# Kernel optimization log

Measured on AMD Instinct MI355X. Metric: run time of the kernel, lower is better.

Reference implementation:

```python
import jax, jax.numpy as jnp
import numpy as np

LOWER_T = 6.0
UPPER_T = 50.0


def _conv(x, w, pad_h, pad_w):
    # x: [N,1,H,W] or [N,Cin,H,W]; w: [O,I,kh,kw]; cross-correlation like torch Conv2d
    return jax.lax.conv_general_dilated(
        x, w, window_strides=(1, 1),
        padding=[(pad_h, pad_h), (pad_w, pad_w)],
        dimension_numbers=('NCHW', 'OIHW', 'NCHW'))


def setup_inputs() -> dict:
    key = jax.random.key(0)
    H = W = 4096
    img = jax.random.uniform(key, (1, 3, H, W), dtype=jnp.float32) * 255.0

    # scipy.signal.gaussian(5, std=1.0), unnormalized window
    std = 1.0
    g = np.exp(-0.5 * ((np.arange(5, dtype=np.float32) - 2.0) / std) ** 2).astype(np.float32)
    gauss = jnp.asarray(g)  # [5]

    sobel = jnp.asarray(np.array([[1, 0, -1], [2, 0, -2], [1, 0, -1]], dtype=np.float32))  # [3,3]

    f = np.zeros((8, 1, 3, 3), dtype=np.float32)
    f[:, 0, 1, 1] = 1.0
    offs = [(1, 2), (2, 2), (2, 1), (2, 0), (1, 0), (0, 0), (0, 1), (0, 2)]  # 0,45,...,315 deg
    for k, (r, c) in enumerate(offs):
        f[k, 0, r, c] = -1.0
    dir_w = jnp.asarray(f)  # [8,1,3,3]

    return {"img": img, "gauss": gauss, "sobel": sobel, "dir_w": dir_w}


def reference(img, gauss, sobel, dir_w):
    N, C, H, W = img.shape  # N == 1, C == 3
    x = img.reshape(C, 1, H, W)  # treat channels as batch

    # separable gaussian blur: 1x5 then 5x1, padding 2 (matches torch Conv2d)
    gw_h = gauss.reshape(1, 1, 1, 5)
    gw_v = gauss.reshape(1, 1, 5, 1)
    blurred = _conv(_conv(x, gw_h, 0, 2), gw_v, 2, 0)  # [3,1,H,W]

    sw_h = sobel.reshape(1, 1, 3, 3)
    sw_v = sobel.T.reshape(1, 1, 3, 3)
    gx = _conv(blurred, sw_h, 1, 1)  # [3,1,H,W]
    gy = _conv(blurred, sw_v, 1, 1)

    # per-channel magnitude summed over RGB -> [1,1,H,W]
    grad_mag = jnp.sqrt(gx * gx + gy * gy + 1e-8).sum(axis=0, keepdims=True)[:, 0:1]

    gx_sum = gx.sum(axis=0, keepdims=True)[:, 0:1]
    gy_sum = gy.sum(axis=0, keepdims=True)[:, 0:1]
    ori = jnp.arctan2(gy_sum, gx_sum) * (180.0 / 3.14159) + 180.0
    ori = jnp.round(ori / 45.0) * 45.0

    all_filtered = _conv(grad_mag, dir_w, 1, 1)  # [1,8,H,W]

    idx_pos = jnp.mod(ori / 45.0, 8.0).astype(jnp.int32)          # [1,1,H,W]
    idx_neg = jnp.mod(ori / 45.0 + 4.0, 8.0).astype(jnp.int32)

    cs_pos = jnp.take_along_axis(all_filtered, idx_pos, axis=1)  # [1,1,H,W]
    cs_neg = jnp.take_along_axis(all_filtered, idx_neg, axis=1)

    is_max = jnp.minimum(cs_pos, cs_neg) > 0.0

    thin = jnp.where(is_max, grad_mag, 0.0)
    keep = is_max & (thin >= LOWER_T) & (thin <= UPPER_T)
    thresholded = jnp.where(keep, 1.0, 0.0).astype(jnp.float32)  # [1,1,H,W]
    return thresholded
```

## Files before the change

### kernel.cpp

```cpp
#include <hip/hip_runtime.h>


#define IMG_H 4096
#define IMG_W 4096

constexpr int TW = 32, TH = 32;
constexpr int HBH = 40, HBW = 40;
constexpr int BH  = 36, BW  = 40;
constexpr int MH  = 34, MW  = 36;

__global__ __launch_bounds__(256, 6)
void canny_fused(const float* __restrict__ img,
                 const float* __restrict__ gauss,
                 float* __restrict__ out) {
  __shared__ float s_hb[HBH * HBW];
  __shared__ float s_bl[BH * BW];
  __shared__ float s_bs[BH * BW];
  __shared__ float s_mg[MH * MW];

  const int tid = threadIdx.x;
  const int X0 = blockIdx.x * TW;
  const int Y0 = blockIdx.y * TH;

  const float g0 = gauss[0], g1 = gauss[1], g2 = gauss[2],
              g3 = gauss[3], g4 = gauss[4];

  for (int ch = 0; ch < 3; ++ch) {
    const float* im = img + (size_t)ch * ((size_t)IMG_H * IMG_W);

    for (int j = tid; j < HBH * 10; j += 256) {
      int r = j / 10, g = j - r * 10;
      int c0 = g * 4;
      int gy = Y0 - 4 + r;
      float4 o;
      if ((unsigned)gy < IMG_H) {
        int cb = X0 - 4 + c0;
        const float* row = im + (size_t)gy * IMG_W;
        float a0, a1, a2, a3, a4, a5, a6, a7;
        if (cb >= 0 && cb + 7 < IMG_W) {
          float4 va = *(const float4*)(row + cb);
          float4 vb = *(const float4*)(row + cb + 4);
          a0 = va.x; a1 = va.y; a2 = va.z; a3 = va.w;
          a4 = vb.x; a5 = vb.y; a6 = vb.z; a7 = vb.w;
        } else {
          float t[8];
#pragma unroll
          for (int u = 0; u < 8; ++u) {
            int x = cb + u;
            t[u] = ((unsigned)x < IMG_W) ? row[x] : 0.f;
          }
          a0 = t[0]; a1 = t[1]; a2 = t[2]; a3 = t[3];
          a4 = t[4]; a5 = t[5]; a6 = t[6]; a7 = t[7];
        }
        o.x = g0 * a0 + g1 * a1 + g2 * a2 + g3 * a3 + g4 * a4;
        o.y = g0 * a1 + g1 * a2 + g2 * a3 + g3 * a4 + g4 * a5;
        o.z = g0 * a2 + g1 * a3 + g2 * a4 + g3 * a5 + g4 * a6;
        o.w = g0 * a3 + g1 * a4 + g2 * a5 + g3 * a6 + g4 * a7;
      } else {
        o = make_float4(0.f, 0.f, 0.f, 0.f);
      }
      *(float4*)&s_hb[r * HBW + c0] = o;
    }
    __syncthreads();

    for (int j = tid; j < BH * 10; j += 256) {
      int r = j / 10, g = j - r * 10;
      int c0 = g * 4;
      float4 a0 = *(const float4*)&s_hb[(r    ) * HBW + c0];
      float4 a1 = *(const float4*)&s_hb[(r + 1) * HBW + c0];
      float4 a2 = *(const float4*)&s_hb[(r + 2) * HBW + c0];
      float4 a3 = *(const float4*)&s_hb[(r + 3) * HBW + c0];
      float4 a4 = *(const float4*)&s_hb[(r + 4) * HBW + c0];
      float4 v;
      v.x = g0 * a0.x + g1 * a1.x + g2 * a2.x + g3 * a3.x + g4 * a4.x;
      v.y = g0 * a0.y + g1 * a1.y + g2 * a2.y + g3 * a3.y + g4 * a4.y;
      v.z = g0 * a0.z + g1 * a1.z + g2 * a2.z + g3 * a3.z + g4 * a4.z;
      v.w = g0 * a0.w + g1 * a1.w + g2 * a2.w + g3 * a3.w + g4 * a4.w;
      int gy = Y0 - 2 + r;
      bool rok = (unsigned)gy < IMG_H;
      int gx0 = X0 - 2 + c0;
      v.x = (rok && (unsigned)(gx0    ) < IMG_W) ? v.x : 0.f;
      v.y = (rok && (unsigned)(gx0 + 1) < IMG_W) ? v.y : 0.f;
      v.z = (rok && (unsigned)(gx0 + 2) < IMG_W) ? v.z : 0.f;
      v.w = (rok && (unsigned)(gx0 + 3) < IMG_W) ? v.w : 0.f;
      *(float4*)&s_bl[r * BW + c0] = v;
      float4* ps = (float4*)&s_bs[r * BW + c0];
      if (ch == 0) {
        *ps = v;
      } else {
        float4 s = *ps;
        s.x += v.x; s.y += v.y; s.z += v.z; s.w += v.w;
        *ps = s;
      }
    }
    __syncthreads();

    for (int j = tid; j < MH * 9; j += 256) {
      int r = j / 9, g = j - r * 9;
      int c0 = g * 4;
      float w0[6], w1[6], w2[6];
      {
        float4 p = *(const float4*)&s_bl[(r    ) * BW + c0];
        float2 q = *(const float2*)&s_bl[(r    ) * BW + c0 + 4];
        w0[0]=p.x; w0[1]=p.y; w0[2]=p.z; w0[3]=p.w; w0[4]=q.x; w0[5]=q.y;
      }
      {
        float4 p = *(const float4*)&s_bl[(r + 1) * BW + c0];
        float2 q = *(const float2*)&s_bl[(r + 1) * BW + c0 + 4];
        w1[0]=p.x; w1[1]=p.y; w1[2]=p.z; w1[3]=p.w; w1[4]=q.x; w1[5]=q.y;
      }
      {
        float4 p = *(const float4*)&s_bl[(r + 2) * BW + c0];
        float2 q = *(const float2*)&s_bl[(r + 2) * BW + c0 + 4];
        w2[0]=p.x; w2[1]=p.y; w2[2]=p.z; w2[3]=p.w; w2[4]=q.x; w2[5]=q.y;
      }
      int gy = Y0 - 1 + r;
      bool rok = (unsigned)gy < IMG_H;
      float res[4];
#pragma unroll
      for (int e = 0; e < 4; ++e) {
        float gxv = w0[e] - w0[e + 2] + 2.f * w1[e] - 2.f * w1[e + 2] + w2[e] - w2[e + 2];
        float gyv = w0[e] + 2.f * w0[e + 1] + w0[e + 2] - w2[e] - 2.f * w2[e + 1] - w2[e + 2];
        float m = sqrtf(gxv * gxv + gyv * gyv + 1e-8f);
        int gx = X0 - 1 + c0 + e;
        res[e] = (rok && (unsigned)gx < IMG_W) ? m : 0.f;
      }
      float4* pd = (float4*)&s_mg[r * MW + c0];
      if (ch == 0) {
        *pd = make_float4(res[0], res[1], res[2], res[3]);
      } else {
        float4 s = *pd;
        s.x += res[0]; s.y += res[1]; s.z += res[2]; s.w += res[3];
        *pd = s;
      }
    }
    __syncthreads();
  }

  {
    const int ty  = tid >> 3;
    const int tx0 = (tid & 7) << 2;
    float w0[8], w1[8], w2[8];
#pragma unroll
    for (int rr = 0; rr < 3; ++rr) {
      float* w = (rr == 0) ? w0 : (rr == 1) ? w1 : w2;
      float4 p = *(const float4*)&s_bs[(ty + 1 + rr) * BW + tx0];
      float4 q = *(const float4*)&s_bs[(ty + 1 + rr) * BW + tx0 + 4];
      w[0]=p.x; w[1]=p.y; w[2]=p.z; w[3]=p.w; w[4]=q.x; w[5]=q.y; w[6]=q.z; w[7]=q.w;
    }
    const unsigned long long off_tbl = 0xDDDCDBFF23242501ULL;
    float res[4];
#pragma unroll
    for (int e = 0; e < 4; ++e) {
      int tx = tx0 + e;
      float b00 = w0[e + 1], b01 = w0[e + 2], b02 = w0[e + 3];
      float b10 = w1[e + 1],                  b12 = w1[e + 3];
      float b20 = w2[e + 1], b21 = w2[e + 2], b22 = w2[e + 3];
      float gxs = b00 - b02 + 2.f * b10 - 2.f * b12 + b20 - b22;
      float gys = b00 + 2.f * b01 + b02 - b20 - 2.f * b21 - b22;
      float ori = atan2f(gys, gxs) * 57.295827908797776f + 180.0f;
      int k = (int)rintf(ori / 45.0f);
      int ip = k & 7;
      int off = (int)(signed char)(off_tbl >> (ip * 8));
      int ctr = (ty + 1) * MW + (tx + 1);
      float mc  = s_mg[ctr];
      float csp = mc - s_mg[ctr + off];
      float csn = mc - s_mg[ctr - off];
      bool is_max = fminf(csp, csn) > 0.0f;
      bool keep = is_max && (mc >= 6.0f) && (mc <= 50.0f);
      res[e] = keep ? 1.0f : 0.0f;
    }
    *(float4*)&out[(size_t)(Y0 + ty) * IMG_W + (X0 + tx0)] =
        make_float4(res[0], res[1], res[2], res[3]);
  }
}

extern "C" void kernel_launch(void* const* d_in, const int* in_sizes, int n_in,
                              void* d_out, int out_size, void* d_ws, size_t ws_size,
                              hipStream_t stream) {
  const float* img   = (const float*)d_in[0];
  const float* gauss = (const float*)d_in[1];
  float* out = (float*)d_out;
  dim3 grid(IMG_W / TW, IMG_H / TH);
  canny_fused<<<grid, 256, 0, stream>>>(img, gauss, out);
}
```

Before: 370.9 us.

## Specialize interior tiles and accumulate per-pixel gradient sums in shared memory

Splits the fused Canny kernel into templated interior and border paths, so interior tiles skip all bounds checks and masking. It also drops the blurred-sum buffer and instead accumulates the per-channel Sobel gx/gy into shared arrays, removing the recomputation of gradient sums in the final stage. Per-channel loops are fully unrolled. Shared memory per block grows by one extra 34x36 buffer, which may reduce occupancy, and code size grows because of the two template instantiations.

```diff
diff --git a/kernel.cpp b/kernel.cpp
--- a/kernel.cpp
+++ b/kernel.cpp
@@ -9,15 +9,138 @@
 constexpr int BH  = 36, BW  = 40;
 constexpr int MH  = 34, MW  = 36;
 
+struct Smem {
+  float hb[HBH * HBW];
+  float bl[BH * BW];
+  float mg[MH * MW];
+  float gx[MH * MW];
+  float gy[MH * MW];
+};
+
+template <bool INTERIOR>
+__device__ __forceinline__ void run_stages(Smem& sm, const float* __restrict__ img,
+                                           int X0, int Y0, int tid,
+                                           float g0, float g1, float g2, float g3, float g4) {
+#pragma unroll
+  for (int ch = 0; ch < 3; ++ch) {
+    const float* im = img + (size_t)ch * ((size_t)IMG_H * IMG_W);
+
+    for (int j = tid; j < HBH * 10; j += 256) {
+      int r = j / 10, g = j - r * 10, c0 = g * 4;
+      float4 o;
+      if (INTERIOR) {
+        const float* row = im + (size_t)(Y0 - 4 + r) * IMG_W + (X0 - 4 + c0);
+        float4 va = *(const float4*)row;
+        float4 vb = *(const float4*)(row + 4);
+        o.x = g0*va.x + g1*va.y + g2*va.z + g3*va.w + g4*vb.x;
+        o.y = g0*va.y + g1*va.z + g2*va.w + g3*vb.x + g4*vb.y;
+        o.z = g0*va.z + g1*va.w + g2*vb.x + g3*vb.y + g4*vb.z;
+        o.w = g0*va.w + g1*vb.x + g2*vb.y + g3*vb.z + g4*vb.w;
+      } else {
+        int gy_ = Y0 - 4 + r;
+        if ((unsigned)gy_ < IMG_H) {
+          int cb = X0 - 4 + c0;
+          const float* row = im + (size_t)gy_ * IMG_W;
+          float t[8];
+#pragma unroll
+          for (int u = 0; u < 8; ++u) {
+            int x = cb + u;
+            t[u] = ((unsigned)x < IMG_W) ? row[x] : 0.f;
+          }
+          o.x = g0*t[0] + g1*t[1] + g2*t[2] + g3*t[3] + g4*t[4];
+          o.y = g0*t[1] + g1*t[2] + g2*t[3] + g3*t[4] + g4*t[5];
+          o.z = g0*t[2] + g1*t[3] + g2*t[4] + g3*t[5] + g4*t[6];
+          o.w = g0*t[3] + g1*t[4] + g2*t[5] + g3*t[6] + g4*t[7];
+        } else {
+          o = make_float4(0.f, 0.f, 0.f, 0.f);
+        }
+      }
+      *(float4*)&sm.hb[r * HBW + c0] = o;
+    }
+    __syncthreads();
+
+    for (int j = tid; j < BH * 10; j += 256) {
+      int r = j / 10, g = j - r * 10, c0 = g * 4;
+      float4 a0 = *(const float4*)&sm.hb[(r    ) * HBW + c0];
+      float4 a1 = *(const float4*)&sm.hb[(r + 1) * HBW + c0];
+      float4 a2 = *(const float4*)&sm.hb[(r + 2) * HBW + c0];
+      float4 a3 = *(const float4*)&sm.hb[(r + 3) * HBW + c0];
+      float4 a4 = *(const float4*)&sm.hb[(r + 4) * HBW + c0];
+      float4 v;
+      v.x = g0*a0.x + g1*a1.x + g2*a2.x + g3*a3.x + g4*a4.x;
+      v.y = g0*a0.y + g1*a1.y + g2*a2.y + g3*a3.y + g4*a4.y;
+      v.z = g0*a0.z + g1*a1.z + g2*a2.z + g3*a3.z + g4*a4.z;
+      v.w = g0*a0.w + g1*a1.w + g2*a2.w + g3*a3.w + g4*a4.w;
+      if (!INTERIOR) {
+        int gy_ = Y0 - 2 + r;
+        bool rok = (unsigned)gy_ < IMG_H;
+        int gx0 = X0 - 2 + c0;
+        v.x = (rok && (unsigned)(gx0    ) < IMG_W) ? v.x : 0.f;
+        v.y = (rok && (unsigned)(gx0 + 1) < IMG_W) ? v.y : 0.f;
+        v.z = (rok && (unsigned)(gx0 + 2) < IMG_W) ? v.z : 0.f;
+        v.w = (rok && (unsigned)(gx0 + 3) < IMG_W) ? v.w : 0.f;
+      }
+      *(float4*)&sm.bl[r * BW + c0] = v;
+    }
+    __syncthreads();
+
+    for (int j = tid; j < MH * 9; j += 256) {
+      int r = j / 9, g = j - r * 9, c0 = g * 4;
+      float w0[6], w1[6], w2[6];
+      {
+        float4 p = *(const float4*)&sm.bl[(r    ) * BW + c0];
+        float2 q = *(const float2*)&sm.bl[(r    ) * BW + c0 + 4];
+        w0[0]=p.x; w0[1]=p.y; w0[2]=p.z; w0[3]=p.w; w0[4]=q.x; w0[5]=q.y;
+      }
+      {
+        float4 p = *(const float4*)&sm.bl[(r + 1) * BW + c0];
+        float2 q = *(const float2*)&sm.bl[(r + 1) * BW + c0 + 4];
+        w1[0]=p.x; w1[1]=p.y; w1[2]=p.z; w1[3]=p.w; w1[4]=q.x; w1[5]=q.y;
+      }
+      {
+        float4 p = *(const float4*)&sm.bl[(r + 2) * BW + c0];
+        float2 q = *(const float2*)&sm.bl[(r + 2) * BW + c0 + 4];
+        w2[0]=p.x; w2[1]=p.y; w2[2]=p.z; w2[3]=p.w; w2[4]=q.x; w2[5]=q.y;
+      }
+      float vgx[4], vgy[4], vmg[4];
+#pragma unroll
+      for (int e = 0; e < 4; ++e) {
+        float gxv = w0[e] - w0[e + 2] + 2.f * w1[e] - 2.f * w1[e + 2] + w2[e] - w2[e + 2];
+        float gyv = w0[e] + 2.f * w0[e + 1] + w0[e + 2] - w2[e] - 2.f * w2[e + 1] - w2[e + 2];
+        float m = sqrtf(gxv * gxv + gyv * gyv + 1e-8f);
+        if (!INTERIOR) {
+          int gyy = Y0 - 1 + r, gxx = X0 - 1 + c0 + e;
+          m = ((unsigned)gyy < IMG_H && (unsigned)gxx < IMG_W) ? m : 0.f;
+        }
+        vgx[e] = gxv; vgy[e] = gyv; vmg[e] = m;
+      }
+      int idx = r * MW + c0;
+      if (ch == 0) {
+        *(float4*)&sm.mg[idx] = make_float4(vmg[0], vmg[1], vmg[2], vmg[3]);
+        *(float4*)&sm.gx[idx] = make_float4(vgx[0], vgx[1], vgx[2], vgx[3]);
+        *(float4*)&sm.gy[idx] = make_float4(vgy[0], vgy[1], vgy[2], vgy[3]);
+      } else {
+        float4 s;
+        s = *(float4*)&sm.mg[idx];
+        s.x += vmg[0]; s.y += vmg[1]; s.z += vmg[2]; s.w += vmg[3];
+        *(float4*)&sm.mg[idx] = s;
+        s = *(float4*)&sm.gx[idx];
+        s.x += vgx[0]; s.y += vgx[1]; s.z += vgx[2]; s.w += vgx[3];
+        *(float4*)&sm.gx[idx] = s;
+        s = *(float4*)&sm.gy[idx];
+        s.x += vgy[0]; s.y += vgy[1]; s.z += vgy[2]; s.w += vgy[3];
+        *(float4*)&sm.gy[idx] = s;
+      }
+    }
+    __syncthreads();
+  }
+}
+
 __global__ __launch_bounds__(256, 6)
 void canny_fused(const float* __restrict__ img,
                  const float* __restrict__ gauss,
                  float* __restrict__ out) {
-  __shared__ float s_hb[HBH * HBW];
-  __shared__ float s_bl[BH * BW];
-  __shared__ float s_bs[BH * BW];
-  __shared__ float s_mg[MH * MW];
-
+  __shared__ Smem sm;
   const int tid = threadIdx.x;
   const int X0 = blockIdx.x * TW;
   const int Y0 = blockIdx.y * TH;
@@ -25,154 +148,33 @@
   const float g0 = gauss[0], g1 = gauss[1], g2 = gauss[2],
               g3 = gauss[3], g4 = gauss[4];
 
-  for (int ch = 0; ch < 3; ++ch) {
-    const float* im = img + (size_t)ch * ((size_t)IMG_H * IMG_W);
+  const bool interior = (X0 >= 4) && (X0 + 40 <= IMG_W) &&
+                        (Y0 >= 4) && (Y0 + 36 <= IMG_H);
+  if (interior) run_stages<true>(sm, img, X0, Y0, tid, g0, g1, g2, g3, g4);
+  else          run_stages<false>(sm, img, X0, Y0, tid, g0, g1, g2, g3, g4);
 
-    for (int j = tid; j < HBH * 10; j += 256) {
-      int r = j / 10, g = j - r * 10;
-      int c0 = g * 4;
-      int gy = Y0 - 4 + r;
-      float4 o;
-      if ((unsigned)gy < IMG_H) {
-        int cb = X0 - 4 + c0;
-        const float* row = im + (size_t)gy * IMG_W;
-        float a0, a1, a2, a3, a4, a5, a6, a7;
-        if (cb >= 0 && cb + 7 < IMG_W) {
-          float4 va = *(const float4*)(row + cb);
-          float4 vb = *(const float4*)(row + cb + 4);
-          a0 = va.x; a1 = va.y; a2 = va.z; a3 = va.w;
-          a4 = vb.x; a5 = vb.y; a6 = vb.z; a7 = vb.w;
-        } else {
-          float t[8];
+  const int ty  = tid >> 3;
+  const int tx0 = (tid & 7) << 2;
+  const int base = (ty + 1) * MW + (tx0 + 1);
+  const unsigned long long off_tbl = 0xDDDCDBFF23242501ULL;
+  float res[4];
 #pragma unroll
-          for (int u = 0; u < 8; ++u) {
-            int x = cb + u;
-            t[u] = ((unsigned)x < IMG_W) ? row[x] : 0.f;
-          }
-          a0 = t[0]; a1 = t[1]; a2 = t[2]; a3 = t[3];
-          a4 = t[4]; a5 = t[5]; a6 = t[6]; a7 = t[7];
-        }
-        o.x = g0 * a0 + g1 * a1 + g2 * a2 + g3 * a3 + g4 * a4;
-        o.y = g0 * a1 + g1 * a2 + g2 * a3 + g3 * a4 + g4 * a5;
-        o.z = g0 * a2 + g1 * a3 + g2 * a4 + g3 * a5 + g4 * a6;
-        o.w = g0 * a3 + g1 * a4 + g2 * a5 + g3 * a6 + g4 * a7;
-      } else {
-        o = make_float4(0.f, 0.f, 0.f, 0.f);
-      }
-      *(float4*)&s_hb[r * HBW + c0] = o;
-    }
-    __syncthreads();
-
-    for (int j = tid; j < BH * 10; j += 256) {
-      int r = j / 10, g = j - r * 10;
-      int c0 = g * 4;
-      float4 a0 = *(const float4*)&s_hb[(r    ) * HBW + c0];
-      float4 a1 = *(const float4*)&s_hb[(r + 1) * HBW + c0];
-      float4 a2 = *(const float4*)&s_hb[(r + 2) * HBW + c0];
-      float4 a3 = *(const float4*)&s_hb[(r + 3) * HBW + c0];
-      float4 a4 = *(const float4*)&s_hb[(r + 4) * HBW + c0];
-      float4 v;
-      v.x = g0 * a0.x + g1 * a1.x + g2 * a2.x + g3 * a3.x + g4 * a4.x;
-      v.y = g0 * a0.y + g1 * a1.y + g2 * a2.y + g3 * a3.y + g4 * a4.y;
-      v.z = g0 * a0.z + g1 * a1.z + g2 * a2.z + g3 * a3.z + g4 * a4.z;
-      v.w = g0 * a0.w + g1 * a1.w + g2 * a2.w + g3 * a3.w + g4 * a4.w;
-      int gy = Y0 - 2 + r;
-      bool rok = (unsigned)gy < IMG_H;
-      int gx0 = X0 - 2 + c0;
-      v.x = (rok && (unsigned)(gx0    ) < IMG_W) ? v.x : 0.f;
-      v.y = (rok && (unsigned)(gx0 + 1) < IMG_W) ? v.y : 0.f;
-      v.z = (rok && (unsigned)(gx0 + 2) < IMG_W) ? v.z : 0.f;
-      v.w = (rok && (unsigned)(gx0 + 3) < IMG_W) ? v.w : 0.f;
-      *(float4*)&s_bl[r * BW + c0] = v;
-      float4* ps = (float4*)&s_bs[r * BW + c0];
-      if (ch == 0) {
-        *ps = v;
-      } else {
-        float4 s = *ps;
-        s.x += v.x; s.y += v.y; s.z += v.z; s.w += v.w;
-        *ps = s;
-      }
-    }
-    __syncthreads();
-
-    for (int j = tid; j < MH * 9; j += 256) {
-      int r = j / 9, g = j - r * 9;
-      int c0 = g * 4;
-      float w0[6], w1[6], w2[6];
-      {
-        float4 p = *(const float4*)&s_bl[(r    ) * BW + c0];
-        float2 q = *(const float2*)&s_bl[(r    ) * BW + c0 + 4];
-        w0[0]=p.x; w0[1]=p.y; w0[2]=p.z; w0[3]=p.w; w0[4]=q.x; w0[5]=q.y;
-      }
-      {
-        float4 p = *(const float4*)&s_bl[(r + 1) * BW + c0];
-        float2 q = *(const float2*)&s_bl[(r + 1) * BW + c0 + 4];
-        w1[0]=p.x; w1[1]=p.y; w1[2]=p.z; w1[3]=p.w; w1[4]=q.x; w1[5]=q.y;
-      }
-      {
-        float4 p = *(const float4*)&s_bl[(r + 2) * BW + c0];
-        float2 q = *(const float2*)&s_bl[(r + 2) * BW + c0 + 4];
-        w2[0]=p.x; w2[1]=p.y; w2[2]=p.z; w2[3]=p.w; w2[4]=q.x; w2[5]=q.y;
-      }
-      int gy = Y0 - 1 + r;
-      bool rok = (unsigned)gy < IMG_H;
-      float res[4];
-#pragma unroll
-      for (int e = 0; e < 4; ++e) {
-        float gxv = w0[e] - w0[e + 2] + 2.f * w1[e] - 2.f * w1[e + 2] + w2[e] - w2[e + 2];
-        float gyv = w0[e] + 2.f * w0[e + 1] + w0[e + 2] - w2[e] - 2.f * w2[e + 1] - w2[e + 2];
-        float m = sqrtf(gxv * gxv + gyv * gyv + 1e-8f);
-        int gx = X0 - 1 + c0 + e;
-        res[e] = (rok && (unsigned)gx < IMG_W) ? m : 0.f;
-      }
-      float4* pd = (float4*)&s_mg[r * MW + c0];
-      if (ch == 0) {
-        *pd = make_float4(res[0], res[1], res[2], res[3]);
-      } else {
-        float4 s = *pd;
-        s.x += res[0]; s.y += res[1]; s.z += res[2]; s.w += res[3];
-        *pd = s;
-      }
-    }
-    __syncthreads();
+  for (int e = 0; e < 4; ++e) {
+    float gxs = sm.gx[base + e];
+    float gys = sm.gy[base + e];
+    float mc  = sm.mg[base + e];
+    float ori = atan2f(gys, gxs) * 57.295827908797776f + 180.0f;
+    int k = (int)rintf(ori / 45.0f);
+    int ip = k & 7;
+    int off = (int)(signed char)(off_tbl >> (ip * 8));
+    float csp = mc - sm.mg[base + e + off];
+    float csn = mc - sm.mg[base + e - off];
+    bool is_max = fminf(csp, csn) > 0.0f;
+    bool keep = is_max && (mc >= 6.0f) && (mc <= 50.0f);
+    res[e] = keep ? 1.0f : 0.0f;
   }
-
-  {
-    const int ty  = tid >> 3;
-    const int tx0 = (tid & 7) << 2;
-    float w0[8], w1[8], w2[8];
-#pragma unroll
-    for (int rr = 0; rr < 3; ++rr) {
-      float* w = (rr == 0) ? w0 : (rr == 1) ? w1 : w2;
-      float4 p = *(const float4*)&s_bs[(ty + 1 + rr) * BW + tx0];
-      float4 q = *(const float4*)&s_bs[(ty + 1 + rr) * BW + tx0 + 4];
-      w[0]=p.x; w[1]=p.y; w[2]=p.z; w[3]=p.w; w[4]=q.x; w[5]=q.y; w[6]=q.z; w[7]=q.w;
-    }
-    const unsigned long long off_tbl = 0xDDDCDBFF23242501ULL;
-    float res[4];
-#pragma unroll
-    for (int e = 0; e < 4; ++e) {
-      int tx = tx0 + e;
-      float b00 = w0[e + 1], b01 = w0[e + 2], b02 = w0[e + 3];
-      float b10 = w1[e + 1],                  b12 = w1[e + 3];
-      float b20 = w2[e + 1], b21 = w2[e + 2], b22 = w2[e + 3];
-      float gxs = b00 - b02 + 2.f * b10 - 2.f * b12 + b20 - b22;
-      float gys = b00 + 2.f * b01 + b02 - b20 - 2.f * b21 - b22;
-      float ori = atan2f(gys, gxs) * 57.295827908797776f + 180.0f;
-      int k = (int)rintf(ori / 45.0f);
-      int ip = k & 7;
-      int off = (int)(signed char)(off_tbl >> (ip * 8));
-      int ctr = (ty + 1) * MW + (tx + 1);
-      float mc  = s_mg[ctr];
-      float csp = mc - s_mg[ctr + off];
-      float csn = mc - s_mg[ctr - off];
-      bool is_max = fminf(csp, csn) > 0.0f;
-      bool keep = is_max && (mc >= 6.0f) && (mc <= 50.0f);
-      res[e] = keep ? 1.0f : 0.0f;
-    }
-    *(float4*)&out[(size_t)(Y0 + ty) * IMG_W + (X0 + tx0)] =
-        make_float4(res[0], res[1], res[2], res[3]);
-  }
+  *(float4*)&out[(size_t)(Y0 + ty) * IMG_W + (X0 + tx0)] =
+      make_float4(res[0], res[1], res[2], res[3]);
 }
 
 extern "C" void kernel_launch(void* const* d_in, const int* in_sizes, int n_in,
```

After: 483.9 us. 1.3x slower.
